# Optimization experiments

Hardware: AMD Instinct MI355X
Metric: run time of the kernel (lower is better)

## Reference

```python
import jax, jax.numpy as jnp
from jax import lax
import numpy as np

L = 10          # number of integration steps
B, H, W = 4, 256, 256
HID = 100       # res_block hidden channels
SIGMA = 4.0     # RKHS Gaussian sigma
KSIZE = 25      # Gaussian kernel taps (~6*sigma+1, odd)
MU = 0.02       # residual weighting
SLOPE = 0.01    # LeakyReLU negative slope


def _conv(x, w, padding):
    return lax.conv_general_dilated(x, w, (1, 1), padding,
                                    dimension_numbers=('NCHW', 'OIHW', 'NCHW'))


def _sobel(img):
    # kornia SpatialGradient(mode='sobel'), normalized (L1 norm 8), replicate pad
    sx = jnp.array([[-1., 0., 1.], [-2., 0., 2.], [-1., 0., 1.]], img.dtype) / 8.0
    k = jnp.stack([sx, sx.T])[:, None]                     # [2,1,3,3] -> (dx, dy)
    imp = jnp.pad(img, ((0, 0), (0, 0), (1, 1), (1, 1)), mode='edge')
    return _conv(imp, k, 'VALID')                          # [B,2,H,W]


def _blur(x):
    # GaussianRKHS2d: separable normalized Gaussian, constant(zero) border
    b, c, h, w = x.shape
    r = jnp.arange(KSIZE, dtype=x.dtype) - (KSIZE - 1) / 2
    g = jnp.exp(-0.5 * (r / SIGMA) ** 2)
    g = g / jnp.sum(g)
    p = KSIZE // 2
    xr = x.reshape(b * c, 1, h, w)
    y = _conv(xr, g.reshape(1, 1, KSIZE, 1), [(p, p), (0, 0)])
    y = _conv(y, g.reshape(1, 1, 1, KSIZE), [(0, 0), (p, p)])
    return y.reshape(b, c, h, w)


def _deform(img, grid):
    # grid_sample(bilinear, zeros padding, align_corners=True) with pixel-coord grid (x,y)
    b, c, h, w = img.shape
    x = grid[..., 0]
    y = grid[..., 1]
    x0 = jnp.floor(x)
    y0 = jnp.floor(y)
    wx = x - x0
    wy = y - y0
    ix0 = x0.astype(jnp.int32)
    iy0 = y0.astype(jnp.int32)

    def samp(im, ix0, iy0, wx, wy):
        imf = im.reshape(c, h * w)

        def g(iy, ix):
            valid = ((ix >= 0) & (ix < w) & (iy >= 0) & (iy < h)).astype(im.dtype)
            idx = (jnp.clip(iy, 0, h - 1) * w + jnp.clip(ix, 0, w - 1)).reshape(-1)
            return imf[:, idx].reshape(c, h, w) * valid

        return (g(iy0, ix0) * (1 - wx) * (1 - wy)
                + g(iy0, ix0 + 1) * wx * (1 - wy)
                + g(iy0 + 1, ix0) * (1 - wx) * wy
                + g(iy0 + 1, ix0 + 1) * wx * wy)

    return jax.vmap(samp)(img, ix0, iy0, wx, wy)


def _res_block(z, img, w1, b1, w2):
    x = jnp.concatenate([z, img], axis=1)                  # [B,2,H,W]
    x = _conv(x, w1, 'SAME') + b1[None, :, None, None]
    x = jnp.where(x >= 0, x, SLOPE * x)                    # LeakyReLU
    return _conv(x, w2, 'SAME')                            # [B,1,H,W]


def _id_grid(b, dtype):
    gx, gy = jnp.meshgrid(jnp.arange(W, dtype=dtype), jnp.arange(H, dtype=dtype))
    g = jnp.stack([gx, gy], -1)                            # [H,W,2] (x,y) pixel coords
    return jnp.broadcast_to(g, (b, H, W, 2))


def _forward(source, source_seg, z0, w1, b1, w2):
    b = source.shape[0]
    idg = _id_grid(b, source.dtype)
    image = source
    res0 = jnp.broadcast_to(z0, (b,) + z0.shape[1:])       # [B,1,H,W]
    residuals = [res0]
    rd = res0                                              # residuals_deformed stacked on channel dim
    phi = idg
    fields, grads = [], []
    for i in range(L):
        g2 = _sobel(image)                                 # [B,2,H,W]
        grads.append(g2[:, None])                          # [B,1,2,H,W]
        field = _blur(-residuals[i] * g2).transpose(0, 2, 3, 1)  # [B,H,W,2]
        fields.append(field)
        deformation = idg - field / L
        f = _res_block(residuals[i], image, w1[i], b1[i], w2[i]) / L
        residuals.append(residuals[i] + f)
        rd = _deform(rd, deformation)                      # warp ALL previous residuals
        rd = jnp.concatenate([rd, residuals[-1]], axis=1)
        phi = _deform(phi.transpose(0, 3, 1, 2), deformation).transpose(0, 2, 3, 1)
        mask = _deform(source_seg, phi)
        image = _deform(source, phi) + jnp.sum(rd[:, 1:], axis=1, keepdims=True) * (MU ** 2 / L) * mask
    return image, jnp.stack(fields), jnp.stack(residuals), jnp.stack(grads)


def setup_inputs():
    key = jax.random.key(0)
    ks = jax.random.split(key, 5)
    source = jax.random.uniform(ks[0], (B, 1, H, W), jnp.float32)
    source_seg = jax.random.uniform(ks[1], (B, 1, H, W), jnp.float32)
    z0 = jax.random.normal(ks[2], (1, 1, H, W), jnp.float32) * 0.1
    w1 = jax.random.normal(ks[3], (L, HID, 2, 3, 3), jnp.float32) * 0.1
    b1 = jnp.zeros((L, HID), jnp.float32)
    w2 = jax.random.normal(ks[4], (L, 1, HID, 3, 3), jnp.float32) * 0.1
    return {"source": source, "source_seg": source_seg, "z0": z0,
            "w1": w1, "b1": b1, "w2": w2}


def reference(source, source_seg, z0, w1, b1, w2):
    return _forward(source, source_seg, z0, w1, b1, w2)
```

## Files before the change

### kernel.cpp

```cpp
#include <hip/hip_runtime.h>
#include <math.h>

#define L 10
#define B 4
#define H 256
#define W 256
#define HID 100
#define SIGMA 4.0f
#define KSIZE 25
#define KHALF 12
#define MU 0.02f
#define SLOPE 0.01f
#define HW (H*W)


__device__ __forceinline__ float tap2(const float* __restrict__ im, int y, int x) {
    return (x >= 0 && x < W && y >= 0 && y < H) ? im[y * W + x] : 0.f;
}

__device__ __forceinline__ float bilin(const float* __restrict__ im, float x, float y) {
    float xf = floorf(x), yf = floorf(y);
    int x0 = (int)xf, y0 = (int)yf;
    float wx = x - xf, wy = y - yf;
    float v00 = tap2(im, y0, x0),     v01 = tap2(im, y0, x0 + 1);
    float v10 = tap2(im, y0 + 1, x0), v11 = tap2(im, y0 + 1, x0 + 1);
    return v00 * (1.f - wx) * (1.f - wy) + v01 * wx * (1.f - wy)
         + v10 * (1.f - wx) * wy         + v11 * wx * wy;
}

__device__ __forceinline__ void gaussw(float g[KSIZE]) {
    float s = 0.f;
#pragma unroll
    for (int k = 0; k < KSIZE; ++k) {
        float r = ((float)k - (float)KHALF) * (1.f / SIGMA);
        float v = expf(-0.5f * r * r);
        g[k] = v; s += v;
    }
    float inv = 1.f / s;
#pragma unroll
    for (int k = 0; k < KSIZE; ++k) g[k] *= inv;
}


__global__ void init_kernel(const float* __restrict__ source, const float* __restrict__ z0,
                            float* __restrict__ res0_out, float* __restrict__ rd0,
                            float* __restrict__ phi0, float* __restrict__ image_buf) {
    int idx = blockIdx.x * 256 + threadIdx.x;
    if (idx >= B * HW) return;
    int b = idx / HW, p = idx % HW;
    int y = p / W, x = p % W;
    float z = z0[p];
    res0_out[idx] = z;
    rd0[(size_t)(b * 11 + 0) * HW + p] = z;
    image_buf[idx] = source[idx];
    phi0[(size_t)(b * 2 + 0) * HW + p] = (float)x;
    phi0[(size_t)(b * 2 + 1) * HW + p] = (float)y;
}


__global__ __launch_bounds__(256)
void field_kernel(const float* __restrict__ img, const float* __restrict__ res,
                  float* __restrict__ grads_l, float* __restrict__ field_l) {
    __shared__ float s_img[58][59];
    __shared__ float s_t[2][56][57];
    __shared__ float s_vb[2][32][57];

    const int tid = threadIdx.x;
    const int b = blockIdx.z;
    const int TY0 = blockIdx.y * 32, TX0 = blockIdx.x * 32;
    const float* imb = img + (size_t)b * HW;
    const float* reb = res + (size_t)b * HW;

    for (int q = tid; q < 58 * 58; q += 256) {
        int sy = q / 58, sx = q % 58;
        int gy = min(max(TY0 - 13 + sy, 0), H - 1);
        int gx = min(max(TX0 - 13 + sx, 0), W - 1);
        s_img[sy][sx] = imb[gy * W + gx];
    }
    __syncthreads();

    for (int q = tid; q < 56 * 56; q += 256) {
        int py = q / 56, px = q % 56;
        int sy = py + 1, sx = px + 1;
        float a00 = s_img[sy-1][sx-1], a01 = s_img[sy-1][sx], a02 = s_img[sy-1][sx+1];
        float a10 = s_img[sy  ][sx-1],                         a12 = s_img[sy  ][sx+1];
        float a20 = s_img[sy+1][sx-1], a21 = s_img[sy+1][sx], a22 = s_img[sy+1][sx+1];
        float dx = (a02 - a00 + 2.f * (a12 - a10) + a22 - a20) * 0.125f;
        float dy = (a20 - a00 + 2.f * (a21 - a01) + a22 - a02) * 0.125f;
        int gy = TY0 - 12 + py, gx = TX0 - 12 + px;
        bool in = ((unsigned)gy < H) && ((unsigned)gx < W);
        float rv = in ? reb[gy * W + gx] : 0.f;
        s_t[0][py][px] = in ? -rv * dx : 0.f;
        s_t[1][py][px] = in ? -rv * dy : 0.f;
        if (py >= 12 && py < 44 && px >= 12 && px < 44) {
            grads_l[(size_t)(b * 2 + 0) * HW + gy * W + gx] = dx;
            grads_l[(size_t)(b * 2 + 1) * HW + gy * W + gx] = dy;
        }
    }
    __syncthreads();

    float g[KSIZE]; gaussw(g);

    for (int q = tid; q < 2 * 32 * 56; q += 256) {
        int ch = q / (32 * 56), r = q % (32 * 56);
        int vy = r / 56, vx = r % 56;
        float acc = 0.f;
#pragma unroll
        for (int k = 0; k < KSIZE; ++k) acc = fmaf(g[k], s_t[ch][vy + k][vx], acc);
        s_vb[ch][vy][vx] = acc;
    }
    __syncthreads();

    for (int q = tid; q < 2 * 32 * 32; q += 256) {
        int ch = q / 1024, p = q % 1024;
        int hy = p / 32, hx = p % 32;
        float acc = 0.f;
#pragma unroll
        for (int k = 0; k < KSIZE; ++k) acc = fmaf(g[k], s_vb[ch][hy][hx + k], acc);
        field_l[((size_t)(b * H + TY0 + hy) * W + TX0 + hx) * 2 + ch] = acc;
    }
}


__global__ __launch_bounds__(256, 4)
void resblock_kernel(const float* __restrict__ res_i, const float* __restrict__ img,
                     const float* __restrict__ w1, const float* __restrict__ b1,
                     const float* __restrict__ w2, float* __restrict__ part) {
    __shared__ float s_in[2][20][21];
    __shared__ float2 s_hid[5][18][20];

    const int tid = threadIdx.x;
    const int z = blockIdx.z;
    const int b = z & 3;
    const int g = z >> 2;
    const int TY0 = blockIdx.y * 16, TX0 = blockIdx.x * 16;

    for (int q = tid; q < 20 * 20; q += 256) {
        int ry = q / 20, rx = q % 20;
        int gy = TY0 - 2 + ry, gx = TX0 - 2 + rx;
        bool v = ((unsigned)gy < H) && ((unsigned)gx < W);
        size_t gp = (size_t)b * HW + gy * W + gx;
        s_in[0][ry][rx] = v ? res_i[gp] : 0.f;
        s_in[1][ry][rx] = v ? img[gp]   : 0.f;
    }
    __syncthreads();

    const int qq  = (tid < 162) ? tid : 161;
    const int hy  = qq / 9, hx2 = (qq % 9) * 2;
    const int gy1 = TY0 - 1 + hy, gx0 = TX0 - 1 + hx2;
    const bool gyok = ((unsigned)gy1 < H);
    const bool in0 = gyok && ((unsigned)gx0 < W);
    const bool in1 = gyok && ((unsigned)(gx0 + 1) < W);

    float xv[2][3][4];
#pragma unroll
    for (int ic = 0; ic < 2; ++ic)
#pragma unroll
        for (int j = 0; j < 3; ++j)
#pragma unroll
            for (int i = 0; i < 4; ++i)
                xv[ic][j][i] = s_in[ic][hy + j][hx2 + i];

    const int ty = tid >> 4, tx = tid & 15;
    float acc = 0.f;

#pragma unroll 1
    for (int cc = 0; cc < 5; ++cc) {
        if (tid < 162) {
#pragma unroll 1
            for (int k = 0; k < 5; ++k) {
                int chA = g * 50 + cc * 10 + 2 * k;
                const float* wpA = w1 + chA * 18;
                const float* wpB = wpA + 18;
                float bA = b1[chA], bB = b1[chA + 1];
                float a0 = bA, a1 = bA, c0 = bB, c1 = bB;
#pragma unroll
                for (int ic = 0; ic < 2; ++ic)
#pragma unroll
                    for (int j = 0; j < 3; ++j)
#pragma unroll
                        for (int i = 0; i < 3; ++i) {
                            float wA = wpA[ic * 9 + j * 3 + i];
                            float wB = wpB[ic * 9 + j * 3 + i];
                            a0 = fmaf(wA, xv[ic][j][i],     a0);
                            a1 = fmaf(wA, xv[ic][j][i + 1], a1);
                            c0 = fmaf(wB, xv[ic][j][i],     c0);
                            c1 = fmaf(wB, xv[ic][j][i + 1], c1);
                        }
                a0 = (a0 >= 0.f) ? a0 : SLOPE * a0;
                a1 = (a1 >= 0.f) ? a1 : SLOPE * a1;
                c0 = (c0 >= 0.f) ? c0 : SLOPE * c0;
                c1 = (c1 >= 0.f) ? c1 : SLOPE * c1;
                float4 wv;
                wv.x = in0 ? a0 : 0.f;  wv.y = in0 ? c0 : 0.f;
                wv.z = in1 ? a1 : 0.f;  wv.w = in1 ? c1 : 0.f;
                *(float4*)&s_hid[k][hy][hx2] = wv;
            }
        }
        __syncthreads();

#pragma unroll 1
        for (int k = 0; k < 5; ++k) {
            const float* wqA = w2 + (g * 50 + cc * 10 + 2 * k) * 9;
            const float* wqB = wqA + 9;
#pragma unroll
            for (int j = 0; j < 3; ++j) {
                float2 v0 = s_hid[k][ty + j][tx + 0];
                float2 v1 = s_hid[k][ty + j][tx + 1];
                float2 v2 = s_hid[k][ty + j][tx + 2];
                acc = fmaf(wqA[j * 3 + 0], v0.x, acc);
                acc = fmaf(wqB[j * 3 + 0], v0.y, acc);
                acc = fmaf(wqA[j * 3 + 1], v1.x, acc);
                acc = fmaf(wqB[j * 3 + 1], v1.y, acc);
                acc = fmaf(wqA[j * 3 + 2], v2.x, acc);
                acc = fmaf(wqB[j * 3 + 2], v2.y, acc);
            }
        }
        __syncthreads();
    }

    size_t gp = (size_t)b * HW + (TY0 + ty) * W + TX0 + tx;
    part[(size_t)g * (B * HW) + gp] = acc;
}


__global__ void efg_kernel(const float* __restrict__ field,
                           const float* __restrict__ res_prev,
                           const float* __restrict__ part,
                           float* __restrict__ res_next,
                           const float* __restrict__ rd_old, float* __restrict__ rd_new,
                           int nc_old,
                           const float* __restrict__ phi_old, float* __restrict__ phi_new,
                           const float* __restrict__ seg, const float* __restrict__ source,
                           float* __restrict__ image_buf, float* __restrict__ image_out) {
    int idx = blockIdx.x * 256 + threadIdx.x;
    if (idx >= B * HW) return;
    int b = idx / HW, p = idx % HW;
    int y = p / W, x = p % W;

    float rn = res_prev[idx] + (part[idx] + part[(size_t)B * HW + idx]) * (1.f / (float)L);
    res_next[idx] = rn;

    float fx = field[((size_t)(b * HW + p)) * 2 + 0];
    float fy = field[((size_t)(b * HW + p)) * 2 + 1];
    float sx = (float)x - fx * (1.f / (float)L);
    float sy = (float)y - fy * (1.f / (float)L);

    float xf = floorf(sx), yf = floorf(sy);
    int x0 = (int)xf, y0 = (int)yf;
    float wx = sx - xf, wy = sy - yf;
    float mx0 = (x0 >= 0 && x0 < W) ? 1.f : 0.f;
    float mx1 = (x0 + 1 >= 0 && x0 + 1 < W) ? 1.f : 0.f;
    float my0 = (y0 >= 0 && y0 < H) ? 1.f : 0.f;
    float my1 = (y0 + 1 >= 0 && y0 + 1 < H) ? 1.f : 0.f;
    float W00 = (1.f - wx) * (1.f - wy) * mx0 * my0;
    float W01 = wx * (1.f - wy) * mx1 * my0;
    float W10 = (1.f - wx) * wy * mx0 * my1;
    float W11 = wx * wy * mx1 * my1;
    int xc0 = min(max(x0, 0), W - 1), xc1 = min(max(x0 + 1, 0), W - 1);
    int yc0 = min(max(y0, 0), H - 1), yc1 = min(max(y0 + 1, 0), H - 1);
    int o00 = yc0 * W + xc0, o01 = yc0 * W + xc1;
    int o10 = yc1 * W + xc0, o11 = yc1 * W + xc1;

    float s = 0.f;
    for (int c = 0; c < nc_old; ++c) {
        const float* im = rd_old + (size_t)(b * 11 + c) * HW;
        float v = W00 * im[o00] + W01 * im[o01] + W10 * im[o10] + W11 * im[o11];
        rd_new[(size_t)(b * 11 + c) * HW + p] = v;
        if (c > 0) s += v;
    }
    rd_new[(size_t)(b * 11 + nc_old) * HW + p] = rn;
    s += rn;

    const float* phx = phi_old + (size_t)(b * 2 + 0) * HW;
    const float* phy = phi_old + (size_t)(b * 2 + 1) * HW;
    float pxn = W00 * phx[o00] + W01 * phx[o01] + W10 * phx[o10] + W11 * phx[o11];
    float pyn = W00 * phy[o00] + W01 * phy[o01] + W10 * phy[o10] + W11 * phy[o11];
    phi_new[(size_t)(b * 2 + 0) * HW + p] = pxn;
    phi_new[(size_t)(b * 2 + 1) * HW + p] = pyn;

    float mask = bilin(seg + (size_t)b * HW, pxn, pyn);
    float sw   = bilin(source + (size_t)b * HW, pxn, pyn);
    float img = sw + s * (MU * MU / (float)L) * mask;
    image_buf[idx] = img;
    image_out[idx] = img;
}


extern "C" void kernel_launch(void* const* d_in, const int* in_sizes, int n_in,
                              void* d_out, int out_size, void* d_ws, size_t ws_size,
                              hipStream_t stream) {
    const float* source = (const float*)d_in[0];
    const float* seg    = (const float*)d_in[1];
    const float* z0     = (const float*)d_in[2];
    const float* w1     = (const float*)d_in[3];
    const float* b1     = (const float*)d_in[4];
    const float* w2     = (const float*)d_in[5];
    float* out = (float*)d_out;

    const size_t nPix = (size_t)B * HW;
    float* out_image  = out;
    float* out_fields = out + nPix;
    float* out_res    = out_fields + (size_t)L * nPix * 2;
    float* out_grads  = out_res + (size_t)(L + 1) * nPix;

    float* ws        = (float*)d_ws;
    float* image_buf = ws;
    float* part_buf  = image_buf + nPix;
    float* phi_buf0  = part_buf + 2 * nPix;
    float* phi_buf1  = phi_buf0 + 2 * nPix;
    float* rd_buf0   = phi_buf1 + 2 * nPix;
    float* rd_buf1   = rd_buf0 + 11 * nPix;
    float* phi_buf[2] = { phi_buf0, phi_buf1 };
    float* rd_buf[2]  = { rd_buf0, rd_buf1 };

    dim3 blk(256);
    int gPix = (int)((nPix + 255) / 256);

    init_kernel<<<gPix, blk, 0, stream>>>(source, z0, out_res, rd_buf[0], phi_buf[0], image_buf);

    int cur = 0;
    for (int i = 0; i < L; ++i) {
        dim3 gF(W / 32, H / 32, B);
        field_kernel<<<gF, 256, 0, stream>>>(image_buf, out_res + (size_t)i * nPix,
                                             out_grads + (size_t)i * 2 * nPix,
                                             out_fields + (size_t)i * 2 * nPix);
        dim3 gD(W / 16, H / 16, 2 * B);
        resblock_kernel<<<gD, 256, 0, stream>>>(out_res + (size_t)i * nPix, image_buf,
                                                w1 + (size_t)i * HID * 18,
                                                b1 + (size_t)i * HID,
                                                w2 + (size_t)i * HID * 9,
                                                part_buf);
        efg_kernel<<<gPix, blk, 0, stream>>>(out_fields + (size_t)i * 2 * nPix,
                                             out_res + (size_t)i * nPix,
                                             part_buf,
                                             out_res + (size_t)(i + 1) * nPix,
                                             rd_buf[cur], rd_buf[cur ^ 1], i + 1,
                                             phi_buf[cur], phi_buf[cur ^ 1],
                                             seg, source, image_buf, out_image);
        cur ^= 1;
    }
}
```

Before: 551.0 us.

## Widen resblock tile to 16x32 with register blocking of four hidden columns

The residual-block kernel tile grows from 16x16 to 16x32 output pixels per block. Each first-stage thread now computes four adjacent hidden-layer columns for two channels, and each second-stage thread produces two outputs using float4 shared-memory reads and a float2 store. The aim is to cut halo recomputation overhead and the number of weight loads per output. The cost is more registers and shared memory per block and half as many blocks in the grid.

```diff
diff --git a/kernel.cpp b/kernel.cpp
--- a/kernel.cpp
+++ b/kernel.cpp
@@ -126,17 +126,17 @@
 void resblock_kernel(const float* __restrict__ res_i, const float* __restrict__ img,
                      const float* __restrict__ w1, const float* __restrict__ b1,
                      const float* __restrict__ w2, float* __restrict__ part) {
-    __shared__ float s_in[2][20][21];
-    __shared__ float2 s_hid[5][18][20];
+    __shared__ float  s_in[2][20][38];
+    __shared__ float2 s_hid[5][18][36];
 
     const int tid = threadIdx.x;
     const int z = blockIdx.z;
     const int b = z & 3;
     const int g = z >> 2;
-    const int TY0 = blockIdx.y * 16, TX0 = blockIdx.x * 16;
-
-    for (int q = tid; q < 20 * 20; q += 256) {
-        int ry = q / 20, rx = q % 20;
+    const int TY0 = blockIdx.y * 16, TX0 = blockIdx.x * 32;
+
+    for (int q = tid; q < 20 * 36; q += 256) {
+        int ry = q / 36, rx = q % 36;
         int gy = TY0 - 2 + ry, gx = TX0 - 2 + rx;
         bool v = ((unsigned)gy < H) && ((unsigned)gx < W);
         size_t gp = (size_t)b * HW + gy * W + gx;
@@ -146,23 +146,25 @@
     __syncthreads();
 
     const int qq  = (tid < 162) ? tid : 161;
-    const int hy  = qq / 9, hx2 = (qq % 9) * 2;
-    const int gy1 = TY0 - 1 + hy, gx0 = TX0 - 1 + hx2;
+    const int hy  = qq / 9, hq = (qq % 9) * 4;
+    const int gy1 = TY0 - 1 + hy, gx0 = TX0 - 1 + hq;
     const bool gyok = ((unsigned)gy1 < H);
-    const bool in0 = gyok && ((unsigned)gx0 < W);
-    const bool in1 = gyok && ((unsigned)(gx0 + 1) < W);
-
-    float xv[2][3][4];
+    bool inm[4];
+#pragma unroll
+    for (int m = 0; m < 4; ++m) inm[m] = gyok && ((unsigned)(gx0 + m) < W);
+
+    float xv[2][3][6];
 #pragma unroll
     for (int ic = 0; ic < 2; ++ic)
 #pragma unroll
         for (int j = 0; j < 3; ++j)
 #pragma unroll
-            for (int i = 0; i < 4; ++i)
-                xv[ic][j][i] = s_in[ic][hy + j][hx2 + i];
-
-    const int ty = tid >> 4, tx = tid & 15;
-    float acc = 0.f;
+            for (int i = 0; i < 6; ++i)
+                xv[ic][j][i] = s_in[ic][hy + j][hq + i];
+
+    const int ty = tid >> 4;
+    const int c0 = (tid & 15) * 2;
+    float acc0 = 0.f, acc1 = 0.f;
 
 #pragma unroll 1
     for (int cc = 0; cc < 5; ++cc) {
@@ -173,7 +175,8 @@
                 const float* wpA = w1 + chA * 18;
                 const float* wpB = wpA + 18;
                 float bA = b1[chA], bB = b1[chA + 1];
-                float a0 = bA, a1 = bA, c0 = bB, c1 = bB;
+                float a0 = bA, a1 = bA, a2 = bA, a3 = bA;
+                float e0 = bB, e1 = bB, e2 = bB, e3 = bB;
 #pragma unroll
                 for (int ic = 0; ic < 2; ++ic)
 #pragma unroll
@@ -184,17 +187,24 @@
                             float wB = wpB[ic * 9 + j * 3 + i];
                             a0 = fmaf(wA, xv[ic][j][i],     a0);
                             a1 = fmaf(wA, xv[ic][j][i + 1], a1);
-                            c0 = fmaf(wB, xv[ic][j][i],     c0);
-                            c1 = fmaf(wB, xv[ic][j][i + 1], c1);
+                            a2 = fmaf(wA, xv[ic][j][i + 2], a2);
+                            a3 = fmaf(wA, xv[ic][j][i + 3], a3);
+                            e0 = fmaf(wB, xv[ic][j][i],     e0);
+                            e1 = fmaf(wB, xv[ic][j][i + 1], e1);
+                            e2 = fmaf(wB, xv[ic][j][i + 2], e2);
+                            e3 = fmaf(wB, xv[ic][j][i + 3], e3);
                         }
-                a0 = (a0 >= 0.f) ? a0 : SLOPE * a0;
-                a1 = (a1 >= 0.f) ? a1 : SLOPE * a1;
-                c0 = (c0 >= 0.f) ? c0 : SLOPE * c0;
-                c1 = (c1 >= 0.f) ? c1 : SLOPE * c1;
-                float4 wv;
-                wv.x = in0 ? a0 : 0.f;  wv.y = in0 ? c0 : 0.f;
-                wv.z = in1 ? a1 : 0.f;  wv.w = in1 ? c1 : 0.f;
-                *(float4*)&s_hid[k][hy][hx2] = wv;
+                a0 = (a0 >= 0.f) ? a0 : SLOPE * a0;  a1 = (a1 >= 0.f) ? a1 : SLOPE * a1;
+                a2 = (a2 >= 0.f) ? a2 : SLOPE * a2;  a3 = (a3 >= 0.f) ? a3 : SLOPE * a3;
+                e0 = (e0 >= 0.f) ? e0 : SLOPE * e0;  e1 = (e1 >= 0.f) ? e1 : SLOPE * e1;
+                e2 = (e2 >= 0.f) ? e2 : SLOPE * e2;  e3 = (e3 >= 0.f) ? e3 : SLOPE * e3;
+                float4 w01, w23;
+                w01.x = inm[0] ? a0 : 0.f;  w01.y = inm[0] ? e0 : 0.f;
+                w01.z = inm[1] ? a1 : 0.f;  w01.w = inm[1] ? e1 : 0.f;
+                w23.x = inm[2] ? a2 : 0.f;  w23.y = inm[2] ? e2 : 0.f;
+                w23.z = inm[3] ? a3 : 0.f;  w23.w = inm[3] ? e3 : 0.f;
+                *(float4*)&s_hid[k][hy][hq]     = w01;
+                *(float4*)&s_hid[k][hy][hq + 2] = w23;
             }
         }
         __syncthreads();
@@ -205,22 +215,24 @@
             const float* wqB = wqA + 9;
 #pragma unroll
             for (int j = 0; j < 3; ++j) {
-                float2 v0 = s_hid[k][ty + j][tx + 0];
-                float2 v1 = s_hid[k][ty + j][tx + 1];
-                float2 v2 = s_hid[k][ty + j][tx + 2];
-                acc = fmaf(wqA[j * 3 + 0], v0.x, acc);
-                acc = fmaf(wqB[j * 3 + 0], v0.y, acc);
-                acc = fmaf(wqA[j * 3 + 1], v1.x, acc);
-                acc = fmaf(wqB[j * 3 + 1], v1.y, acc);
-                acc = fmaf(wqA[j * 3 + 2], v2.x, acc);
-                acc = fmaf(wqB[j * 3 + 2], v2.y, acc);
+                float4 r0 = *(float4*)&s_hid[k][ty + j][c0];
+                float4 r1 = *(float4*)&s_hid[k][ty + j][c0 + 2];
+                float wA0 = wqA[j * 3 + 0], wA1 = wqA[j * 3 + 1], wA2 = wqA[j * 3 + 2];
+                float wB0 = wqB[j * 3 + 0], wB1 = wqB[j * 3 + 1], wB2 = wqB[j * 3 + 2];
+                acc0 = fmaf(wA0, r0.x, acc0); acc0 = fmaf(wB0, r0.y, acc0);
+                acc0 = fmaf(wA1, r0.z, acc0); acc0 = fmaf(wB1, r0.w, acc0);
+                acc0 = fmaf(wA2, r1.x, acc0); acc0 = fmaf(wB2, r1.y, acc0);
+                acc1 = fmaf(wA0, r0.z, acc1); acc1 = fmaf(wB0, r0.w, acc1);
+                acc1 = fmaf(wA1, r1.x, acc1); acc1 = fmaf(wB1, r1.y, acc1);
+                acc1 = fmaf(wA2, r1.z, acc1); acc1 = fmaf(wB2, r1.w, acc1);
             }
         }
         __syncthreads();
     }
 
-    size_t gp = (size_t)b * HW + (TY0 + ty) * W + TX0 + tx;
-    part[(size_t)g * (B * HW) + gp] = acc;
+    size_t gp = (size_t)b * HW + (TY0 + ty) * W + TX0 + c0;
+    float2 o; o.x = acc0; o.y = acc1;
+    *(float2*)&part[(size_t)g * (B * HW) + gp] = o;
 }
 
 
@@ -325,7 +337,7 @@
         field_kernel<<<gF, 256, 0, stream>>>(image_buf, out_res + (size_t)i * nPix,
                                              out_grads + (size_t)i * 2 * nPix,
                                              out_fields + (size_t)i * 2 * nPix);
-        dim3 gD(W / 16, H / 16, 2 * B);
+        dim3 gD(W / 32, H / 16, 2 * B);
         resblock_kernel<<<gD, 256, 0, stream>>>(out_res + (size_t)i * nPix, image_buf,
                                                 w1 + (size_t)i * HID * 18,
                                                 b1 + (size_t)i * HID,
```

Result: slower. 610.8 us (+10.9%).

## Double-buffer resblock hidden tile to halve barriers between conv stages

Applied to the files above, without the earlier changes.

Doubles the shared hidden-channel buffer so the first conv for the next channel chunk is written while the second conv reads the current chunk, leaving one barrier per chunk instead of two. This cuts synchronisation stalls and lets the 162 conv1 threads and the idle threads overlap their work. In exchange, shared memory per block roughly doubles, which may lower occupancy under the 4-blocks launch bound.

```diff
diff --git a/kernel.cpp b/kernel.cpp
--- a/kernel.cpp
+++ b/kernel.cpp
@@ -126,8 +126,8 @@
 void resblock_kernel(const float* __restrict__ res_i, const float* __restrict__ img,
                      const float* __restrict__ w1, const float* __restrict__ b1,
                      const float* __restrict__ w2, float* __restrict__ part) {
-    __shared__ float s_in[2][20][21];
-    __shared__ float2 s_hid[5][18][20];
+    __shared__ float  s_in[2][20][21];
+    __shared__ float2 s_hid[2][5][18][20];
 
     const int tid = threadIdx.x;
     const int z = blockIdx.z;
@@ -164,60 +164,69 @@
     const int ty = tid >> 4, tx = tid & 15;
     float acc = 0.f;
 
+#define CONV1_CHUNK(cc, buf)                                                  \
+    if (tid < 162) {                                                          \
+        _Pragma("unroll 1")                                                   \
+        for (int k = 0; k < 5; ++k) {                                         \
+            int chA = g * 50 + (cc) * 10 + 2 * k;                             \
+            const float* wpA = w1 + chA * 18;                                 \
+            const float* wpB = wpA + 18;                                      \
+            float bA = b1[chA], bB = b1[chA + 1];                             \
+            float a0 = bA, a1 = bA, c0 = bB, c1 = bB;                         \
+            _Pragma("unroll")                                                 \
+            for (int ic = 0; ic < 2; ++ic)                                    \
+                for (int j = 0; j < 3; ++j)                                   \
+                    for (int i = 0; i < 3; ++i) {                             \
+                        float wA = wpA[ic * 9 + j * 3 + i];                   \
+                        float wB = wpB[ic * 9 + j * 3 + i];                   \
+                        a0 = fmaf(wA, xv[ic][j][i],     a0);                  \
+                        a1 = fmaf(wA, xv[ic][j][i + 1], a1);                  \
+                        c0 = fmaf(wB, xv[ic][j][i],     c0);                  \
+                        c1 = fmaf(wB, xv[ic][j][i + 1], c1);                  \
+                    }                                                         \
+            a0 = (a0 >= 0.f) ? a0 : SLOPE * a0;                               \
+            a1 = (a1 >= 0.f) ? a1 : SLOPE * a1;                               \
+            c0 = (c0 >= 0.f) ? c0 : SLOPE * c0;                               \
+            c1 = (c1 >= 0.f) ? c1 : SLOPE * c1;                               \
+            float4 wv;                                                        \
+            wv.x = in0 ? a0 : 0.f;  wv.y = in0 ? c0 : 0.f;                    \
+            wv.z = in1 ? a1 : 0.f;  wv.w = in1 ? c1 : 0.f;                    \
+            *(float4*)&s_hid[buf][k][hy][hx2] = wv;                           \
+        }                                                                     \
+    }
+
+#define CONV2_CHUNK(cc, buf)                                                  \
+    {                                                                         \
+        _Pragma("unroll 1")                                                   \
+        for (int k = 0; k < 5; ++k) {                                         \
+            const float* wqA = w2 + (g * 50 + (cc) * 10 + 2 * k) * 9;         \
+            const float* wqB = wqA + 9;                                       \
+            _Pragma("unroll")                                                 \
+            for (int j = 0; j < 3; ++j) {                                     \
+                float2 v0 = s_hid[buf][k][ty + j][tx + 0];                    \
+                float2 v1 = s_hid[buf][k][ty + j][tx + 1];                    \
+                float2 v2 = s_hid[buf][k][ty + j][tx + 2];                    \
+                acc = fmaf(wqA[j * 3 + 0], v0.x, acc);                        \
+                acc = fmaf(wqB[j * 3 + 0], v0.y, acc);                        \
+                acc = fmaf(wqA[j * 3 + 1], v1.x, acc);                        \
+                acc = fmaf(wqB[j * 3 + 1], v1.y, acc);                        \
+                acc = fmaf(wqA[j * 3 + 2], v2.x, acc);                        \
+                acc = fmaf(wqB[j * 3 + 2], v2.y, acc);                        \
+            }                                                                 \
+        }                                                                     \
+    }
+
+    CONV1_CHUNK(0, 0)
+    __syncthreads();
+
 #pragma unroll 1
-    for (int cc = 0; cc < 5; ++cc) {
-        if (tid < 162) {
-#pragma unroll 1
-            for (int k = 0; k < 5; ++k) {
-                int chA = g * 50 + cc * 10 + 2 * k;
-                const float* wpA = w1 + chA * 18;
-                const float* wpB = wpA + 18;
-                float bA = b1[chA], bB = b1[chA + 1];
-                float a0 = bA, a1 = bA, c0 = bB, c1 = bB;
-#pragma unroll
-                for (int ic = 0; ic < 2; ++ic)
-#pragma unroll
-                    for (int j = 0; j < 3; ++j)
-#pragma unroll
-                        for (int i = 0; i < 3; ++i) {
-                            float wA = wpA[ic * 9 + j * 3 + i];
-                            float wB = wpB[ic * 9 + j * 3 + i];
-                            a0 = fmaf(wA, xv[ic][j][i],     a0);
-                            a1 = fmaf(wA, xv[ic][j][i + 1], a1);
-                            c0 = fmaf(wB, xv[ic][j][i],     c0);
-                            c1 = fmaf(wB, xv[ic][j][i + 1], c1);
-                        }
-                a0 = (a0 >= 0.f) ? a0 : SLOPE * a0;
-                a1 = (a1 >= 0.f) ? a1 : SLOPE * a1;
-                c0 = (c0 >= 0.f) ? c0 : SLOPE * c0;
-                c1 = (c1 >= 0.f) ? c1 : SLOPE * c1;
-                float4 wv;
-                wv.x = in0 ? a0 : 0.f;  wv.y = in0 ? c0 : 0.f;
-                wv.z = in1 ? a1 : 0.f;  wv.w = in1 ? c1 : 0.f;
-                *(float4*)&s_hid[k][hy][hx2] = wv;
-            }
-        }
+    for (int cc = 0; cc < 4; ++cc) {
+        const int cur = cc & 1, nxt = cur ^ 1;
+        CONV1_CHUNK(cc + 1, nxt)
+        CONV2_CHUNK(cc, cur)
         __syncthreads();
-
-#pragma unroll 1
-        for (int k = 0; k < 5; ++k) {
-            const float* wqA = w2 + (g * 50 + cc * 10 + 2 * k) * 9;
-            const float* wqB = wqA + 9;
-#pragma unroll
-            for (int j = 0; j < 3; ++j) {
-                float2 v0 = s_hid[k][ty + j][tx + 0];
-                float2 v1 = s_hid[k][ty + j][tx + 1];
-                float2 v2 = s_hid[k][ty + j][tx + 2];
-                acc = fmaf(wqA[j * 3 + 0], v0.x, acc);
-                acc = fmaf(wqB[j * 3 + 0], v0.y, acc);
-                acc = fmaf(wqA[j * 3 + 1], v1.x, acc);
-                acc = fmaf(wqB[j * 3 + 1], v1.y, acc);
-                acc = fmaf(wqA[j * 3 + 2], v2.x, acc);
-                acc = fmaf(wqB[j * 3 + 2], v2.y, acc);
-            }
-        }
-        __syncthreads();
-    }
+    }
+    CONV2_CHUNK(4, 0)
 
     size_t gp = (size_t)b * HW + (TY0 + ty) * W + TX0 + tx;
     part[(size_t)g * (B * HW) + gp] = acc;
```

New measurement: 705.8 us. 1.28x slower.

## Scatter hidden activations into per-tap partial sums to remove staged shared-memory conv

Applied to the files above, without the earlier changes.

The second 3x3 conv of the res block is restructured. Each hidden-pixel thread now multiplies its LeakyReLU activations by all 9 output taps, accumulating them in 18 registers across all 50 channels of its group. A single shared-memory write and one barrier follow, and each output pixel then sums 9 shifted partials. This removes the 10 per-chunk barriers and repeated shared loads and stores of hidden activations. In exchange, all 256 threads now run the conv1 work, including the clamped duplicate threads, and register pressure rises.

```diff
diff --git a/kernel.cpp b/kernel.cpp
--- a/kernel.cpp
+++ b/kernel.cpp
@@ -127,7 +127,7 @@
                      const float* __restrict__ w1, const float* __restrict__ b1,
                      const float* __restrict__ w2, float* __restrict__ part) {
     __shared__ float s_in[2][20][21];
-    __shared__ float2 s_hid[5][18][20];
+    __shared__ float s_T[9][324];
 
     const int tid = threadIdx.x;
     const int z = blockIdx.z;
@@ -161,63 +161,65 @@
             for (int i = 0; i < 4; ++i)
                 xv[ic][j][i] = s_in[ic][hy + j][hx2 + i];
 
+    float T0[9], T1[9];
+#pragma unroll
+    for (int t = 0; t < 9; ++t) { T0[t] = 0.f; T1[t] = 0.f; }
+
+#pragma unroll 1
+    for (int cp = 0; cp < 25; ++cp) {
+        const int chA = g * 50 + cp * 2;
+        const float* wpA = w1 + chA * 18;
+        const float* wpB = wpA + 18;
+        float bA = b1[chA], bB = b1[chA + 1];
+        float a0 = bA, a1 = bA, c0 = bB, c1 = bB;
+#pragma unroll
+        for (int ic = 0; ic < 2; ++ic)
+#pragma unroll
+            for (int j = 0; j < 3; ++j)
+#pragma unroll
+                for (int i = 0; i < 3; ++i) {
+                    float wA = wpA[ic * 9 + j * 3 + i];
+                    float wB = wpB[ic * 9 + j * 3 + i];
+                    a0 = fmaf(wA, xv[ic][j][i],     a0);
+                    a1 = fmaf(wA, xv[ic][j][i + 1], a1);
+                    c0 = fmaf(wB, xv[ic][j][i],     c0);
+                    c1 = fmaf(wB, xv[ic][j][i + 1], c1);
+                }
+        a0 = (a0 >= 0.f) ? a0 : SLOPE * a0;
+        a1 = (a1 >= 0.f) ? a1 : SLOPE * a1;
+        c0 = (c0 >= 0.f) ? c0 : SLOPE * c0;
+        c1 = (c1 >= 0.f) ? c1 : SLOPE * c1;
+        a0 = in0 ? a0 : 0.f;  c0 = in0 ? c0 : 0.f;
+        a1 = in1 ? a1 : 0.f;  c1 = in1 ? c1 : 0.f;
+        const float* wqA = w2 + chA * 9;
+        const float* wqB = wqA + 9;
+#pragma unroll
+        for (int t = 0; t < 9; ++t) {
+            float vA = wqA[t], vB = wqB[t];
+            T0[t] = fmaf(vA, a0, T0[t]);
+            T0[t] = fmaf(vB, c0, T0[t]);
+            T1[t] = fmaf(vA, a1, T1[t]);
+            T1[t] = fmaf(vB, c1, T1[t]);
+        }
+    }
+
+    if (tid < 162) {
+        const int pos = hy * 18 + hx2;
+#pragma unroll
+        for (int t = 0; t < 9; ++t) {
+            float2 wv; wv.x = T0[t]; wv.y = T1[t];
+            *(float2*)&s_T[t][pos] = wv;
+        }
+    }
+    __syncthreads();
+
     const int ty = tid >> 4, tx = tid & 15;
     float acc = 0.f;
-
-#pragma unroll 1
-    for (int cc = 0; cc < 5; ++cc) {
-        if (tid < 162) {
-#pragma unroll 1
-            for (int k = 0; k < 5; ++k) {
-                int chA = g * 50 + cc * 10 + 2 * k;
-                const float* wpA = w1 + chA * 18;
-                const float* wpB = wpA + 18;
-                float bA = b1[chA], bB = b1[chA + 1];
-                float a0 = bA, a1 = bA, c0 = bB, c1 = bB;
-#pragma unroll
-                for (int ic = 0; ic < 2; ++ic)
-#pragma unroll
-                    for (int j = 0; j < 3; ++j)
-#pragma unroll
-                        for (int i = 0; i < 3; ++i) {
-                            float wA = wpA[ic * 9 + j * 3 + i];
-                            float wB = wpB[ic * 9 + j * 3 + i];
-                            a0 = fmaf(wA, xv[ic][j][i],     a0);
-                            a1 = fmaf(wA, xv[ic][j][i + 1], a1);
-                            c0 = fmaf(wB, xv[ic][j][i],     c0);
-                            c1 = fmaf(wB, xv[ic][j][i + 1], c1);
-                        }
-                a0 = (a0 >= 0.f) ? a0 : SLOPE * a0;
-                a1 = (a1 >= 0.f) ? a1 : SLOPE * a1;
-                c0 = (c0 >= 0.f) ? c0 : SLOPE * c0;
-                c1 = (c1 >= 0.f) ? c1 : SLOPE * c1;
-                float4 wv;
-                wv.x = in0 ? a0 : 0.f;  wv.y = in0 ? c0 : 0.f;
-                wv.z = in1 ? a1 : 0.f;  wv.w = in1 ? c1 : 0.f;
-                *(float4*)&s_hid[k][hy][hx2] = wv;
-            }
-        }
-        __syncthreads();
-
-#pragma unroll 1
-        for (int k = 0; k < 5; ++k) {
-            const float* wqA = w2 + (g * 50 + cc * 10 + 2 * k) * 9;
-            const float* wqB = wqA + 9;
-#pragma unroll
-            for (int j = 0; j < 3; ++j) {
-                float2 v0 = s_hid[k][ty + j][tx + 0];
-                float2 v1 = s_hid[k][ty + j][tx + 1];
-                float2 v2 = s_hid[k][ty + j][tx + 2];
-                acc = fmaf(wqA[j * 3 + 0], v0.x, acc);
-                acc = fmaf(wqB[j * 3 + 0], v0.y, acc);
-                acc = fmaf(wqA[j * 3 + 1], v1.x, acc);
-                acc = fmaf(wqB[j * 3 + 1], v1.y, acc);
-                acc = fmaf(wqA[j * 3 + 2], v2.x, acc);
-                acc = fmaf(wqB[j * 3 + 2], v2.y, acc);
-            }
-        }
-        __syncthreads();
-    }
+#pragma unroll
+    for (int j = 0; j < 3; ++j)
+#pragma unroll
+        for (int i = 0; i < 3; ++i)
+            acc += s_T[j * 3 + i][(ty + j) * 18 + (tx + i)];
 
     size_t gp = (size_t)b * HW + (TY0 + ty) * W + TX0 + tx;
     part[(size_t)g * (B * HW) + gp] = acc;
```

Result: slower. 595.3 us (+8.0%).
